# Kernel tuning notes

Measured on AMD Instinct MI355X. Metric: run time of the kernel, lower is better.

Reference implementation:

```python
import jax, jax.numpy as jnp
import numpy as np

B, N, F_IN, F_OUT = 64, 1024, 200, 200
NEG_SLOPE = 0.2  # PyG GATConv default


def setup_inputs() -> dict:
    key = jax.random.key(0)
    k1, k2, k3, k4, k5 = jax.random.split(key, 5)
    return {
        "x": jax.random.normal(k1, (B, 1, N, F_IN), dtype=jnp.float32),
        "W": jax.random.normal(k2, (F_IN, F_OUT), dtype=jnp.float32) * 0.05,
        "att_src": jax.random.normal(k3, (F_OUT,), dtype=jnp.float32) * 0.05,
        "att_dst": jax.random.normal(k4, (F_OUT,), dtype=jnp.float32) * 0.05,
        "bias": jax.random.normal(k5, (F_OUT,), dtype=jnp.float32) * 0.05,
    }


def reference(x, W, att_src, att_dst, bias):
    # x: [B, 1, N, F_IN]; module flattens to (B*N) nodes but the edge_index
    # only spans node ids 0..N-1 (complete graph minus self loops). PyG's
    # GATConv re-adds self loops for ALL B*N nodes, so:
    #   nodes 0..N-1 : dense softmax attention over all N nodes (incl. self)
    #   nodes >= N   : only the self loop -> out = h_i + bias
    b, _, n, f = x.shape
    xf = x.reshape(b * n, f)
    h = xf @ W                                # [B*N, F_OUT] linear transform

    h0 = h[:n]                                # first graph's nodes
    a_s = h0 @ att_src                        # [N] per-source score
    a_d = h0 @ att_dst                        # [N] per-target score
    # score[i, j] = leaky_relu(a_dst[i] + a_src[j]), softmax over sources j
    scores = jax.nn.leaky_relu(a_d[:, None] + a_s[None, :], negative_slope=NEG_SLOPE)
    alpha = jax.nn.softmax(scores, axis=1)    # [N, N]
    out0 = alpha @ h0 + bias                  # [N, F_OUT]

    out_rest = h[n:] + bias                   # self-loop only -> alpha == 1
    out = jnp.concatenate([out0, out_rest], axis=0)
    return out.reshape(b, n, -1)[:, None]     # [B, 1, N, F_OUT]
```

## Files before the change

kernel.cpp:

```cpp
#include <hip/hip_runtime.h>

#define BATCH 64
#define NNODE 1024
#define FDIM  200
#define MROWS (BATCH * NNODE)
#define NEG_SLOPE 0.2f

#define NKT 7
#define NNT 13
#define NTP 7
#define FRAGW_BYTES (NKT * NNT * 1024)
#define NBLK 256

typedef short s16x8 __attribute__((ext_vector_type(8)));
typedef float f32x4 __attribute__((ext_vector_type(4)));


__device__ __forceinline__ unsigned int f2bf(float f) {
    unsigned int u = __float_as_uint(f);
    return (u + 0x7fffu + ((u >> 16) & 1u)) >> 16;
}
__device__ __forceinline__ unsigned int pack2(float a, float b) {
    return f2bf(a) | (f2bf(b) << 16);
}
__device__ __forceinline__ float lrelu(float s) {
    return (s > 0.f) ? s : NEG_SLOPE * s;
}

__global__ __launch_bounds__(64) void k_prep(const float* __restrict__ W,
                                             const float* __restrict__ att_src,
                                             const float* __restrict__ att_dst,
                                             unsigned short* __restrict__ fragW,
                                             float* __restrict__ wsv,
                                             float* __restrict__ wdv)
{
    const int b    = blockIdx.x;
    const int lane = threadIdx.x;

    if (b < 91) {
        const int kt   = b / NNT;
        const int nt   = b - kt * NNT;
        const int n    = nt * 16 + (lane & 15);
        const int kb   = kt * 32 + (lane >> 4) * 8;
        s16x8 v;
        #pragma unroll
        for (int j = 0; j < 8; ++j) {
            int k = kb + j;
            float f = (k < FDIM && n < FDIM) ? W[k * FDIM + n] : 0.f;
            v[j] = (short)f2bf(f);
        }
        ((s16x8*)(fragW + (size_t)b * 512))[lane] = v;
    } else {
        const int kk = b - 91;
        const float* Wr = W + kk * FDIM;
        float ps = 0.f, pd = 0.f;
        #pragma unroll
        for (int i = 0; i < 4; ++i) {
            int n = lane + i * 64;
            if (n < FDIM) {
                float wv = Wr[n];
                ps = fmaf(wv, att_src[n], ps);
                pd = fmaf(wv, att_dst[n], pd);
            }
        }
        #pragma unroll
        for (int off = 32; off; off >>= 1) {
            ps += __shfl_down(ps, off);
            pd += __shfl_down(pd, off);
        }
        if (lane == 0) { wsv[kk] = ps; wdv[kk] = pd; }
    }
}

__global__ __launch_bounds__(512, 2) void k_gemm(const float* __restrict__ x,
                                                 const unsigned short* __restrict__ fragW,
                                                 const float* __restrict__ bias,
                                                 const float* __restrict__ wsv,
                                                 const float* __restrict__ wdv,
                                                 float* __restrict__ out,
                                                 unsigned short* __restrict__ h0frag,
                                                 float* __restrict__ a_s,
                                                 float* __restrict__ a_d)
{
    __shared__ __align__(16) unsigned short Bf[FRAGW_BYTES / 2];
    __shared__ float scr[8][16 * 17];
    const int tid  = threadIdx.x;
    const int lane = tid & 63;
    const int w    = __builtin_amdgcn_readfirstlane(tid >> 6);
    const int ln   = lane & 15;
    const int quad = lane >> 4;
    const int row0 = blockIdx.x * 128 + w * 16;
    const int row1 = (blockIdx.x + NBLK) * 128 + w * 16;

    {
        const char* gsrc = (const char*)fragW;
        char* ldst = (char*)&Bf[0];
        #pragma unroll
        for (int r = 0; r < 12; ++r) {
            int off = tid * 16 + r * 8192;
            if (off < FRAGW_BYTES)
                __builtin_amdgcn_global_load_lds(
                    (const __attribute__((address_space(1))) void*)(gsrc + off),
                    (__attribute__((address_space(3))) void*)(ldst + off),
                    16, 0, 0);
        }
    }

    const float* xrow0 = x + (size_t)(row0 + ln) * FDIM;
    const float* xrow1 = x + (size_t)(row1 + ln) * FDIM;
    float4 ar[NKT][2];
    #pragma unroll
    for (int kt = 0; kt < NKT; ++kt) {
        if (kt < 6) {
            const float4* ap = (const float4*)(xrow0 + kt * 32 + quad * 8);
            ar[kt][0] = ap[0]; ar[kt][1] = ap[1];
        } else if (quad == 0) {
            const float4* ap = (const float4*)(xrow0 + kt * 32);
            ar[kt][0] = ap[0]; ar[kt][1] = ap[1];
        } else {
            ar[kt][0] = make_float4(0.f, 0.f, 0.f, 0.f);
            ar[kt][1] = make_float4(0.f, 0.f, 0.f, 0.f);
        }
    }

    f32x4 acc[NNT];
    #pragma unroll
    for (int nt = 0; nt < NNT; ++nt) acc[nt] = (f32x4){0.f, 0.f, 0.f, 0.f};

    __syncthreads();

    float4 ar2[NKT][2];
    #pragma unroll
    for (int kt = 0; kt < NKT; ++kt) {
        if (kt < 6) {
            const float4* ap = (const float4*)(xrow1 + kt * 32 + quad * 8);
            ar2[kt][0] = ap[0]; ar2[kt][1] = ap[1];
        } else if (quad == 0) {
            const float4* ap = (const float4*)(xrow1 + kt * 32);
            ar2[kt][0] = ap[0]; ar2[kt][1] = ap[1];
        } else {
            ar2[kt][0] = make_float4(0.f, 0.f, 0.f, 0.f);
            ar2[kt][1] = make_float4(0.f, 0.f, 0.f, 0.f);
        }
    }

    #pragma unroll
    for (int kt = 0; kt < NKT; ++kt) {
        float4 f0 = ar[kt][0], f1 = ar[kt][1];
        unsigned int au[4] = {pack2(f0.x, f0.y), pack2(f0.z, f0.w),
                              pack2(f1.x, f1.y), pack2(f1.z, f1.w)};
        s16x8 a = *(s16x8*)au;
        const unsigned short* bbase = &Bf[kt * NNT * 512];
        #pragma unroll
        for (int nt = 0; nt < NNT; ++nt) {
            s16x8 b = *(const s16x8*)(bbase + nt * 512 + lane * 8);
            acc[nt] = __builtin_amdgcn_mfma_f32_16x16x32_bf16(a, b, acc[nt], 0, 0, 0);
        }
    }

    if (row0 >= NNODE) {
        #pragma unroll
        for (int nt = 0; nt < NNT; ++nt) {
            int col = nt * 16 + ln;
            if (nt < 12 || ln < 8) {
                float bv = bias[col];
                #pragma unroll
                for (int r = 0; r < 4; ++r)
                    out[(size_t)(row0 + quad * 4 + r) * FDIM + col] = acc[nt][r] + bv;
            }
        }
    } else {
        {
            float ps = 0.f, pd = 0.f;
            #pragma unroll
            for (int kt = 0; kt < NKT; ++kt) {
                if (kt < 6 || quad == 0) {
                    float4 f0 = ar[kt][0], f1 = ar[kt][1];
                    const float4* sp = (const float4*)(wsv + kt * 32 + quad * 8);
                    const float4* dp = (const float4*)(wdv + kt * 32 + quad * 8);
                    float4 s0 = sp[0], s1 = sp[1], d0 = dp[0], d1 = dp[1];
                    ps += f0.x*s0.x + f0.y*s0.y + f0.z*s0.z + f0.w*s0.w
                        + f1.x*s1.x + f1.y*s1.y + f1.z*s1.z + f1.w*s1.w;
                    pd += f0.x*d0.x + f0.y*d0.y + f0.z*d0.z + f0.w*d0.w
                        + f1.x*d1.x + f1.y*d1.y + f1.z*d1.z + f1.w*d1.w;
                }
            }
            ps += __shfl_down(ps, 32); ps += __shfl_down(ps, 16);
            pd += __shfl_down(pd, 32); pd += __shfl_down(pd, 16);
            if (lane < 16) {
                a_s[row0 + lane] = ps;
                a_d[row0 + lane] = pd;
            }
        }
        float* scrw = &scr[w][0];
        const int kt2 = row0 >> 5;
        const int lo  = (row0 >> 4) & 1;
        for (int nt = 0; nt < NNT; ++nt) {
            #pragma unroll
            for (int r = 0; r < 4; ++r) scrw[(quad * 4 + r) * 17 + ln] = acc[nt][r];
            __syncthreads();
            if (lane < 32) {
                int oct = lane >> 4, nl = lane & 15;
                uint4 dv;
                dv.x = pack2(scrw[(oct * 8 + 0) * 17 + nl], scrw[(oct * 8 + 1) * 17 + nl]);
                dv.y = pack2(scrw[(oct * 8 + 2) * 17 + nl], scrw[(oct * 8 + 3) * 17 + nl]);
                dv.z = pack2(scrw[(oct * 8 + 4) * 17 + nl], scrw[(oct * 8 + 5) * 17 + nl]);
                dv.w = pack2(scrw[(oct * 8 + 6) * 17 + nl], scrw[(oct * 8 + 7) * 17 + nl]);
                *(uint4*)(h0frag + ((size_t)(kt2 * NNT + nt) * 64 + lo * 32 + lane) * 8) = dv;
            }
            __syncthreads();
        }
    }

    #pragma unroll
    for (int nt = 0; nt < NNT; ++nt) acc[nt] = (f32x4){0.f, 0.f, 0.f, 0.f};

    #pragma unroll
    for (int kt = 0; kt < NKT; ++kt) {
        float4 f0 = ar2[kt][0], f1 = ar2[kt][1];
        unsigned int au[4] = {pack2(f0.x, f0.y), pack2(f0.z, f0.w),
                              pack2(f1.x, f1.y), pack2(f1.z, f1.w)};
        s16x8 a = *(s16x8*)au;
        const unsigned short* bbase = &Bf[kt * NNT * 512];
        #pragma unroll
        for (int nt = 0; nt < NNT; ++nt) {
            s16x8 b = *(const s16x8*)(bbase + nt * 512 + lane * 8);
            acc[nt] = __builtin_amdgcn_mfma_f32_16x16x32_bf16(a, b, acc[nt], 0, 0, 0);
        }
    }

    #pragma unroll
    for (int nt = 0; nt < NNT; ++nt) {
        int col = nt * 16 + ln;
        if (nt < 12 || ln < 8) {
            float bv = bias[col];
            #pragma unroll
            for (int r = 0; r < 4; ++r)
                out[(size_t)(row1 + quad * 4 + r) * FDIM + col] = acc[nt][r] + bv;
        }
    }
}

__global__ __launch_bounds__(256) void k_attn(const unsigned short* __restrict__ h0frag,
                                              const float* __restrict__ a_s,
                                              const float* __restrict__ a_d,
                                              const float* __restrict__ bias,
                                              float* __restrict__ out)
{
    __shared__ __align__(16) float as_s[1024];
    __shared__ float mls[16];
    __shared__ float rls[16];
    __shared__ f32x4 red[2][3][64];
    const int tid  = threadIdx.x;
    const int lane = tid & 63;
    const int w    = __builtin_amdgcn_readfirstlane(tid >> 6);
    const int ln   = lane & 15;
    const int quad = lane >> 4;
    const int it   = blockIdx.x / NTP;
    const int p    = blockIdx.x - it * NTP;
    const int nt0  = p * 2;
    const int nt1  = p * 2 + 1;
    const bool has1 = (nt1 < NNT);
    const int i0   = it * 16;

    #pragma unroll
    for (int i = 0; i < 4; ++i) as_s[tid + i * 256] = a_s[tid + i * 256];
    __syncthreads();

    float mx = -1e30f;
    #pragma unroll
    for (int i = 0; i < 16; ++i) mx = fmaxf(mx, as_s[lane + i * 64]);
    #pragma unroll
    for (int off = 32; off; off >>= 1) mx = fmaxf(mx, __shfl_down(mx, off));
    mx = __shfl(mx, 0);

    #pragma unroll
    for (int rr = 0; rr < 4; ++rr) {
        const int r  = w * 4 + rr;
        const float adr = a_d[i0 + r];
        const float mi  = lrelu(adr + mx);
        float sum = 0.f;
        #pragma unroll
        for (int i = 0; i < 16; ++i)
            sum += __expf(lrelu(adr + as_s[lane + i * 64]) - mi);
        #pragma unroll
        for (int off = 32; off; off >>= 1) sum += __shfl_down(sum, off);
        if (lane == 0) { mls[r] = mi; rls[r] = 1.0f / sum; }
    }
    __syncthreads();

    const float ad = a_d[i0 + ln];
    const float mi = mls[ln];

    f32x4 acc0A = (f32x4){0.f, 0.f, 0.f, 0.f};
    f32x4 acc0B = (f32x4){0.f, 0.f, 0.f, 0.f};
    f32x4 acc1A = (f32x4){0.f, 0.f, 0.f, 0.f};
    f32x4 acc1B = (f32x4){0.f, 0.f, 0.f, 0.f};

    #pragma unroll
    for (int k8 = 0; k8 < 8; ++k8) {
        const int kt2 = w * 8 + k8;
        const float4* ap = (const float4*)(as_s + kt2 * 32 + quad * 8);
        float4 f0 = ap[0], f1 = ap[1];
        float e[8] = {f0.x, f0.y, f0.z, f0.w, f1.x, f1.y, f1.z, f1.w};
        #pragma unroll
        for (int j = 0; j < 8; ++j)
            e[j] = __expf(lrelu(ad + e[j]) - mi);
        unsigned int au[4] = {pack2(e[0], e[1]), pack2(e[2], e[3]),
                              pack2(e[4], e[5]), pack2(e[6], e[7])};
        s16x8 afrag = *(s16x8*)au;
        const unsigned short* bb = h0frag + ((size_t)(kt2 * NNT + nt0) * 64 + lane) * 8;
        s16x8 b0 = *(const s16x8*)bb;
        if (k8 & 1) acc0B = __builtin_amdgcn_mfma_f32_16x16x32_bf16(afrag, b0, acc0B, 0, 0, 0);
        else        acc0A = __builtin_amdgcn_mfma_f32_16x16x32_bf16(afrag, b0, acc0A, 0, 0, 0);
        if (has1) {
            s16x8 b1 = *(const s16x8*)(bb + 512);
            if (k8 & 1) acc1B = __builtin_amdgcn_mfma_f32_16x16x32_bf16(afrag, b1, acc1B, 0, 0, 0);
            else        acc1A = __builtin_amdgcn_mfma_f32_16x16x32_bf16(afrag, b1, acc1A, 0, 0, 0);
        }
    }

    f32x4 acc0 = acc0A + acc0B;
    f32x4 acc1 = acc1A + acc1B;
    if (w > 0) { red[0][w - 1][lane] = acc0; red[1][w - 1][lane] = acc1; }
    __syncthreads();

    if (w == 0) {
        #pragma unroll
        for (int ww = 0; ww < 3; ++ww) { acc0 += red[0][ww][lane]; acc1 += red[1][ww][lane]; }
        {
            const int col = nt0 * 16 + ln;
            if (nt0 < 12 || ln < 8) {
                float bv = bias[col];
                #pragma unroll
                for (int r = 0; r < 4; ++r) {
                    float rl = rls[quad * 4 + r];
                    out[(size_t)(i0 + quad * 4 + r) * FDIM + col] = acc0[r] * rl + bv;
                }
            }
        }
        if (has1) {
            const int col = nt1 * 16 + ln;
            float bv = bias[col];
            #pragma unroll
            for (int r = 0; r < 4; ++r) {
                float rl = rls[quad * 4 + r];
                out[(size_t)(i0 + quad * 4 + r) * FDIM + col] = acc1[r] * rl + bv;
            }
        }
    }
}

extern "C" void kernel_launch(void* const* d_in, const int* in_sizes, int n_in,
                              void* d_out, int out_size, void* d_ws, size_t ws_size,
                              hipStream_t stream)
{
    const float* x       = (const float*)d_in[0];
    const float* W       = (const float*)d_in[1];
    const float* att_src = (const float*)d_in[2];
    const float* att_dst = (const float*)d_in[3];
    const float* bias    = (const float*)d_in[4];
    float* out = (float*)d_out;
    char*  wsb = (char*)d_ws;

    unsigned short* h0frag = (unsigned short*)(wsb + 0);
    float* a_s   = (float*)(wsb + 425984);
    float* a_d   = (float*)(wsb + 430080);
    unsigned short* fragW = (unsigned short*)(wsb + 442368);
    float* wsv   = (float*)(wsb + 535552);
    float* wdv   = (float*)(wsb + 536352);

    k_prep <<<291,        64, 0, stream>>>(W, att_src, att_dst, fragW, wsv, wdv);
    k_gemm <<<NBLK,      512, 0, stream>>>(x, fragW, bias, wsv, wdv, out, h0frag, a_s, a_d);
    k_attn <<<64 * NTP,  256, 0, stream>>>(h0frag, a_s, a_d, bias, out);
}
```

Baseline: 124.2 us.

## Split GEMM blocks by output-column halves to raise occupancy

The GEMM kernel moves from 256 blocks that each handle two 128-row groups over all 13 column tiles to 1024 blocks that each handle one 128-row group and one half of the column tiles (7 or 6). Each block now loads only its half of the weight fragments into shared memory, which cuts LDS per block, and launch bounds go from 2 to 4 blocks per CU. The aim is more parallelism and occupancy, and fewer registers per thread since the second row set is no longer held. The cost is that every x row is read and converted to bf16 twice, once per column half, and the weight LDS fill is repeated across more blocks.

```diff
diff --git a/kernel.cpp b/kernel.cpp
--- a/kernel.cpp
+++ b/kernel.cpp
@@ -9,8 +9,6 @@
 #define NKT 7
 #define NNT 13
 #define NTP 7
-#define FRAGW_BYTES (NKT * NNT * 1024)
-#define NBLK 256
 
 typedef short s16x8 __attribute__((ext_vector_type(8)));
 typedef float f32x4 __attribute__((ext_vector_type(4)));
@@ -72,50 +70,51 @@
     }
 }
 
-__global__ __launch_bounds__(512, 2) void k_gemm(const float* __restrict__ x,
-                                                 const unsigned short* __restrict__ fragW,
-                                                 const float* __restrict__ bias,
-                                                 const float* __restrict__ wsv,
-                                                 const float* __restrict__ wdv,
-                                                 float* __restrict__ out,
-                                                 unsigned short* __restrict__ h0frag,
-                                                 float* __restrict__ a_s,
-                                                 float* __restrict__ a_d)
-{
-    __shared__ __align__(16) unsigned short Bf[FRAGW_BYTES / 2];
-    __shared__ float scr[8][16 * 17];
-    const int tid  = threadIdx.x;
+template<int NTBASE, int NTLOC>
+__device__ __forceinline__ void gemm_half(const float* __restrict__ x,
+                                          const unsigned short* __restrict__ fragW,
+                                          const float* __restrict__ bias,
+                                          const float* __restrict__ wsv,
+                                          const float* __restrict__ wdv,
+                                          float* __restrict__ out,
+                                          unsigned short* __restrict__ h0frag,
+                                          float* __restrict__ a_s,
+                                          float* __restrict__ a_d,
+                                          unsigned short* Bf, float* scr,
+                                          int rgrp, int tid)
+{
     const int lane = tid & 63;
     const int w    = __builtin_amdgcn_readfirstlane(tid >> 6);
     const int ln   = lane & 15;
     const int quad = lane >> 4;
-    const int row0 = blockIdx.x * 128 + w * 16;
-    const int row1 = (blockIdx.x + NBLK) * 128 + w * 16;
+    const int row0 = rgrp * 128 + w * 16;
 
     {
-        const char* gsrc = (const char*)fragW;
-        char* ldst = (char*)&Bf[0];
-        #pragma unroll
-        for (int r = 0; r < 12; ++r) {
-            int off = tid * 16 + r * 8192;
-            if (off < FRAGW_BYTES)
+        constexpr int NG = NKT * NTLOC;
+        #pragma unroll
+        for (int r = 0; r < (NG + 7) / 8; ++r) {
+            int g = r * 8 + w;
+            if (g < NG) {
+                const int kt = g / NTLOC, nl = g - kt * NTLOC;
+                const char* gsrc = (const char*)fragW
+                    + ((size_t)(kt * NNT + NTBASE + nl)) * 1024 + lane * 16;
+                char* ldst = (char*)Bf + (size_t)g * 1024 + lane * 16;
                 __builtin_amdgcn_global_load_lds(
-                    (const __attribute__((address_space(1))) void*)(gsrc + off),
-                    (__attribute__((address_space(3))) void*)(ldst + off),
-                    16, 0, 0);
-        }
-    }
-
-    const float* xrow0 = x + (size_t)(row0 + ln) * FDIM;
-    const float* xrow1 = x + (size_t)(row1 + ln) * FDIM;
+                    (const __attribute__((address_space(1))) void*)gsrc,
+                    (__attribute__((address_space(3))) void*)ldst, 16, 0, 0);
+            }
+        }
+    }
+
+    const float* xrow = x + (size_t)(row0 + ln) * FDIM;
     float4 ar[NKT][2];
     #pragma unroll
     for (int kt = 0; kt < NKT; ++kt) {
         if (kt < 6) {
-            const float4* ap = (const float4*)(xrow0 + kt * 32 + quad * 8);
+            const float4* ap = (const float4*)(xrow + kt * 32 + quad * 8);
             ar[kt][0] = ap[0]; ar[kt][1] = ap[1];
         } else if (quad == 0) {
-            const float4* ap = (const float4*)(xrow0 + kt * 32);
+            const float4* ap = (const float4*)(xrow + kt * 32);
             ar[kt][0] = ap[0]; ar[kt][1] = ap[1];
         } else {
             ar[kt][0] = make_float4(0.f, 0.f, 0.f, 0.f);
@@ -123,26 +122,11 @@
         }
     }
 
-    f32x4 acc[NNT];
-    #pragma unroll
-    for (int nt = 0; nt < NNT; ++nt) acc[nt] = (f32x4){0.f, 0.f, 0.f, 0.f};
+    f32x4 acc[NTLOC];
+    #pragma unroll
+    for (int nt = 0; nt < NTLOC; ++nt) acc[nt] = (f32x4){0.f, 0.f, 0.f, 0.f};
 
     __syncthreads();
-
-    float4 ar2[NKT][2];
-    #pragma unroll
-    for (int kt = 0; kt < NKT; ++kt) {
-        if (kt < 6) {
-            const float4* ap = (const float4*)(xrow1 + kt * 32 + quad * 8);
-            ar2[kt][0] = ap[0]; ar2[kt][1] = ap[1];
-        } else if (quad == 0) {
-            const float4* ap = (const float4*)(xrow1 + kt * 32);
-            ar2[kt][0] = ap[0]; ar2[kt][1] = ap[1];
-        } else {
-            ar2[kt][0] = make_float4(0.f, 0.f, 0.f, 0.f);
-            ar2[kt][1] = make_float4(0.f, 0.f, 0.f, 0.f);
-        }
-    }
 
     #pragma unroll
     for (int kt = 0; kt < NKT; ++kt) {
@@ -150,19 +134,20 @@
         unsigned int au[4] = {pack2(f0.x, f0.y), pack2(f0.z, f0.w),
                               pack2(f1.x, f1.y), pack2(f1.z, f1.w)};
         s16x8 a = *(s16x8*)au;
-        const unsigned short* bbase = &Bf[kt * NNT * 512];
-        #pragma unroll
-        for (int nt = 0; nt < NNT; ++nt) {
+        const unsigned short* bbase = Bf + kt * NTLOC * 512;
+        #pragma unroll
+        for (int nt = 0; nt < NTLOC; ++nt) {
             s16x8 b = *(const s16x8*)(bbase + nt * 512 + lane * 8);
             acc[nt] = __builtin_amdgcn_mfma_f32_16x16x32_bf16(a, b, acc[nt], 0, 0, 0);
         }
     }
 
-    if (row0 >= NNODE) {
-        #pragma unroll
-        for (int nt = 0; nt < NNT; ++nt) {
-            int col = nt * 16 + ln;
-            if (nt < 12 || ln < 8) {
+    if (rgrp >= 8) {
+        #pragma unroll
+        for (int nt = 0; nt < NTLOC; ++nt) {
+            const int ntg = NTBASE + nt;
+            int col = ntg * 16 + ln;
+            if (ntg < 12 || ln < 8) {
                 float bv = bias[col];
                 #pragma unroll
                 for (int r = 0; r < 4; ++r)
@@ -170,7 +155,7 @@
             }
         }
     } else {
-        {
+        if (NTBASE == 0) {
             float ps = 0.f, pd = 0.f;
             #pragma unroll
             for (int kt = 0; kt < NKT; ++kt) {
@@ -192,10 +177,11 @@
                 a_d[row0 + lane] = pd;
             }
         }
-        float* scrw = &scr[w][0];
+        float* scrw = scr + w * (16 * 17);
         const int kt2 = row0 >> 5;
         const int lo  = (row0 >> 4) & 1;
-        for (int nt = 0; nt < NNT; ++nt) {
+        for (int nt = 0; nt < NTLOC; ++nt) {
+            const int ntg = NTBASE + nt;
             #pragma unroll
             for (int r = 0; r < 4; ++r) scrw[(quad * 4 + r) * 17 + ln] = acc[nt][r];
             __syncthreads();
@@ -206,39 +192,35 @@
                 dv.y = pack2(scrw[(oct * 8 + 2) * 17 + nl], scrw[(oct * 8 + 3) * 17 + nl]);
                 dv.z = pack2(scrw[(oct * 8 + 4) * 17 + nl], scrw[(oct * 8 + 5) * 17 + nl]);
                 dv.w = pack2(scrw[(oct * 8 + 6) * 17 + nl], scrw[(oct * 8 + 7) * 17 + nl]);
-                *(uint4*)(h0frag + ((size_t)(kt2 * NNT + nt) * 64 + lo * 32 + lane) * 8) = dv;
+                *(uint4*)(h0frag + ((size_t)(kt2 * NNT + ntg) * 64 + lo * 32 + lane) * 8) = dv;
             }
             __syncthreads();
         }
     }
-
-    #pragma unroll
-    for (int nt = 0; nt < NNT; ++nt) acc[nt] = (f32x4){0.f, 0.f, 0.f, 0.f};
-
-    #pragma unroll
-    for (int kt = 0; kt < NKT; ++kt) {
-        float4 f0 = ar2[kt][0], f1 = ar2[kt][1];
-        unsigned int au[4] = {pack2(f0.x, f0.y), pack2(f0.z, f0.w),
-                              pack2(f1.x, f1.y), pack2(f1.z, f1.w)};
-        s16x8 a = *(s16x8*)au;
-        const unsigned short* bbase = &Bf[kt * NNT * 512];
-        #pragma unroll
-        for (int nt = 0; nt < NNT; ++nt) {
-            s16x8 b = *(const s16x8*)(bbase + nt * 512 + lane * 8);
-            acc[nt] = __builtin_amdgcn_mfma_f32_16x16x32_bf16(a, b, acc[nt], 0, 0, 0);
-        }
-    }
-
-    #pragma unroll
-    for (int nt = 0; nt < NNT; ++nt) {
-        int col = nt * 16 + ln;
-        if (nt < 12 || ln < 8) {
-            float bv = bias[col];
-            #pragma unroll
-            for (int r = 0; r < 4; ++r)
-                out[(size_t)(row1 + quad * 4 + r) * FDIM + col] = acc[nt][r] + bv;
-        }
-    }
+}
+
+__global__ __launch_bounds__(512, 4) void k_gemm(const float* __restrict__ x,
+                                                 const unsigned short* __restrict__ fragW,
+                                                 const float* __restrict__ bias,
+                                                 const float* __restrict__ wsv,
+                                                 const float* __restrict__ wdv,
+                                                 float* __restrict__ out,
+                                                 unsigned short* __restrict__ h0frag,
+                                                 float* __restrict__ a_s,
+                                                 float* __restrict__ a_d)
+{
+    __shared__ __align__(16) unsigned short Bf[NKT * 7 * 512];
+    __shared__ float scr[8][16 * 17];
+    const int tid  = threadIdx.x;
+    const int rgrp = blockIdx.x >> 1;
+    const int half = blockIdx.x & 1;
+
+    if (half == 0)
+        gemm_half<0, 7>(x, fragW, bias, wsv, wdv, out, h0frag, a_s, a_d,
+                        &Bf[0], &scr[0][0], rgrp, tid);
+    else
+        gemm_half<7, 6>(x, fragW, bias, wsv, wdv, out, h0frag, a_s, a_d,
+                        &Bf[0], &scr[0][0], rgrp, tid);
 }
 
 __global__ __launch_bounds__(256) void k_attn(const unsigned short* __restrict__ h0frag,
@@ -370,7 +352,7 @@
     float* wsv   = (float*)(wsb + 535552);
     float* wdv   = (float*)(wsb + 536352);
 
-    k_prep <<<291,        64, 0, stream>>>(W, att_src, att_dst, fragW, wsv, wdv);
-    k_gemm <<<NBLK,      512, 0, stream>>>(x, fragW, bias, wsv, wdv, out, h0frag, a_s, a_d);
-    k_attn <<<64 * NTP,  256, 0, stream>>>(h0frag, a_s, a_d, bias, out);
-}
+    k_prep <<<291,            64, 0, stream>>>(W, att_src, att_dst, fragW, wsv, wdv);
+    k_gemm <<<MROWS / 64,    512, 0, stream>>>(x, fragW, bias, wsv, wdv, out, h0frag, a_s, a_d);
+    k_attn <<<64 * NTP,      256, 0, stream>>>(h0frag, a_s, a_d, bias, out);
+}
```

Measured after the change: 130.9 us. +5.3%, slower.
